# Kernel tuning notes

Measured on AMD Instinct MI355X. Metric: run time of the kernel, lower is better.

## Reference

```python
import jax, jax.numpy as jnp
import numpy as np
from jax import lax

B, T, L = 2048, 80, 128


def setup_inputs() -> dict:
    key = jax.random.key(0)
    k1, k2, k3, k4, k5 = jax.random.split(key, 5)
    x = jax.random.normal(k1, (B, T, L), dtype=jnp.float32)  # emissions (model logits)
    y = jax.random.randint(k2, (B, T), 0, L)                 # gold tag sequence
    trans = jax.random.normal(k3, (L, L), dtype=jnp.float32) * 0.1
    start_trans = jax.random.normal(k4, (L,), dtype=jnp.float32) * 0.1
    end_trans = jax.random.normal(k5, (L,), dtype=jnp.float32) * 0.1
    return {"x": x, "trans": trans, "start_trans": start_trans,
            "end_trans": end_trans, "y": y}


def reference(x, trans, start_trans, end_trans, y):
    # Linear-chain CRF log-likelihood (TorchCRF semantics, mask = all ones).
    # x: [B,T,L] emissions, y: [B,T] gold tags. Returns [B] log-likelihoods.
    # --- numerator: score of the gold path ---
    emit = jnp.take_along_axis(x, y[..., None], axis=2).squeeze(-1).sum(axis=1)  # [B]
    tr = trans[y[:, :-1], y[:, 1:]].sum(axis=1)                                  # [B]
    numerator = start_trans[y[:, 0]] + emit + tr + end_trans[y[:, -1]]           # [B]
    # --- denominator: log-partition via forward algorithm (scan over time) ---
    alpha0 = start_trans[None, :] + x[:, 0]  # [B,L]
    xt = jnp.swapaxes(x, 0, 1)[1:]           # [T-1,B,L]

    def step(alpha, h_t):
        # alpha[b,i] + trans[i,j] -> logsumexp over i, then add emission h_t[b,j]
        a = jax.nn.logsumexp(alpha[:, :, None] + trans[None, :, :], axis=1) + h_t
        return a, None

    alpha, _ = lax.scan(step, alpha0, xt)
    log_z = jax.nn.logsumexp(alpha + end_trans[None, :], axis=1)  # [B]
    return numerator - log_z
```

## Files before the change

### kernel.cpp

```cpp
#include <hip/hip_runtime.h>
#include <math.h>


#define CRF_B 2048
#define CRF_T 80
#define CRF_L 128

typedef __attribute__((ext_vector_type(8))) short bf16x8_t;
typedef __attribute__((ext_vector_type(4))) float f32x4_t;

union bfrag { bf16x8_t v; unsigned u[4]; unsigned short s[8]; };

__device__ __forceinline__ unsigned pack2(float lo, float hi) {
    return (__float_as_uint(lo) >> 16) | (__float_as_uint(hi) & 0xFFFF0000u);
}
__device__ __forceinline__ unsigned short bft(float f) {
    return (unsigned short)(__float_as_uint(f) >> 16);
}

__global__ __launch_bounds__(64, 1) void crf_v4_kernel(
    const float* __restrict__ x,
    const float* __restrict__ trans,
    const float* __restrict__ start_trans,
    const float* __restrict__ end_trans,
    const int*   __restrict__ y,
    float* __restrict__ out)
{
    const int lane = threadIdx.x;
    const int q    = lane >> 4;
    const int n16  = lane & 15;
    const int row0 = blockIdx.x * 16;
    const int brow = row0 + n16;

    const float* xr = x + (size_t)brow * (CRF_T * CRF_L);

    const int* yb = y + brow * CRF_T;
    float nume = 0.f;
    #pragma unroll
    for (int i = 0; i < 20; ++i) {
        const int t  = 4 * i + q;
        const int yt = yb[t];
        nume += xr[t * CRF_L + yt];
        nume += (t < CRF_T - 1) ? trans[yt * CRF_L + yb[t + 1]] : end_trans[yt];
        if (t == 0) nume += start_trans[yt];
    }
    nume += __shfl_xor(nume, 16);
    nume += __shfl_xor(nume, 32);

    bfrag Af[8][4];
    #pragma unroll
    for (int mt = 0; mt < 8; ++mt) {
        const int m = 16 * mt + n16;
        #pragma unroll
        for (int kk = 0; kk < 4; ++kk) {
            #pragma unroll
            for (int j = 0; j < 8; ++j) {
                const int s = ((2 * kk + (j >> 2)) << 4) | (q << 2) | (j & 3);
                Af[mt][kk].s[j] = bft(__expf(trans[s * CRF_L + m]));
            }
        }
    }

    f32x4_t xA[8], xB[8];
    #pragma unroll
    for (int mt = 0; mt < 8; ++mt) {
        xA[mt] = *(const f32x4_t*)&xr[0 * CRF_L + 16 * mt + 4 * q];
        xB[mt] = *(const f32x4_t*)&xr[1 * CRF_L + 16 * mt + 4 * q];
    }

    bfrag   Bf[4];
    f32x4_t acc[8];
    float crun = 0.f, invM = 1.f;

    #pragma unroll
    for (int mt = 0; mt < 8; ++mt) {
        const f32x4_t st4 = *(const f32x4_t*)&start_trans[16 * mt + 4 * q];
        #pragma unroll
        for (int r = 0; r < 4; ++r)
            acc[mt][r] = __expf(st4[r] + xA[mt][r]);
    }
    #pragma unroll
    for (int mt = 0; mt < 8; ++mt) {
        Bf[mt >> 1].u[2 * (mt & 1) + 0] = pack2(acc[mt][0], acc[mt][1]);
        Bf[mt >> 1].u[2 * (mt & 1) + 1] = pack2(acc[mt][2], acc[mt][3]);
    }
    #pragma unroll
    for (int mt = 0; mt < 8; ++mt)
        xA[mt] = *(const f32x4_t*)&xr[2 * CRF_L + 16 * mt + 4 * q];

    auto step = [&](int t, f32x4_t (&xc)[8]) {
        #pragma unroll
        for (int mt = 0; mt < 8; ++mt) {
            f32x4_t a = {0.f, 0.f, 0.f, 0.f};
            #pragma unroll
            for (int kk = 0; kk < 4; ++kk)
                a = __builtin_amdgcn_mfma_f32_16x16x32_bf16(Af[mt][kk].v, Bf[kk].v, a, 0, 0, 0);
            acc[mt] = a;
        }
        const bool ap = (t & 3) == 0;
        #pragma unroll
        for (int mt = 0; mt < 8; ++mt) {
            #pragma unroll
            for (int r = 0; r < 4; ++r) {
                float e = __expf(xc[mt][r]);
                if (ap) e *= invM;
                acc[mt][r] *= e;
            }
        }
        if (((t & 3) == 3) && (t < CRF_T - 1)) {
            float m = acc[0][0];
            #pragma unroll
            for (int mt = 0; mt < 8; ++mt)
                #pragma unroll
                for (int r = 0; r < 4; ++r)
                    m = fmaxf(m, acc[mt][r]);
            m = fmaxf(m, __shfl_xor(m, 16));
            m = fmaxf(m, __shfl_xor(m, 32));
            crun += __logf(m);
            invM  = 1.0f / m;
        }
        if (t < CRF_T - 1) {
            #pragma unroll
            for (int mt = 0; mt < 8; ++mt) {
                Bf[mt >> 1].u[2 * (mt & 1) + 0] = pack2(acc[mt][0], acc[mt][1]);
                Bf[mt >> 1].u[2 * (mt & 1) + 1] = pack2(acc[mt][2], acc[mt][3]);
            }
        }
        if (t + 2 < CRF_T) {
            #pragma unroll
            for (int mt = 0; mt < 8; ++mt)
                xc[mt] = *(const f32x4_t*)&xr[(t + 2) * CRF_L + 16 * mt + 4 * q];
        }
    };

    for (int tb = 1; tb + 1 < CRF_T; tb += 2) {
        step(tb,     xB);
        step(tb + 1, xA);
    }
    step(CRF_T - 1, xB);

    float sv = 0.f;
    #pragma unroll
    for (int mt = 0; mt < 8; ++mt) {
        const f32x4_t e4 = *(const f32x4_t*)&end_trans[16 * mt + 4 * q];
        #pragma unroll
        for (int r = 0; r < 4; ++r)
            sv += acc[mt][r] * __expf(e4[r]);
    }
    sv += __shfl_xor(sv, 16);
    sv += __shfl_xor(sv, 32);
    if (lane < 16) out[row0 + n16] = nume - (crun + __logf(sv));
}

extern "C" void kernel_launch(void* const* d_in, const int* in_sizes, int n_in,
                              void* d_out, int out_size, void* d_ws, size_t ws_size,
                              hipStream_t stream) {
    const float* x     = (const float*)d_in[0];
    const float* trans = (const float*)d_in[1];
    const float* st    = (const float*)d_in[2];
    const float* et    = (const float*)d_in[3];
    const int*   y     = (const int*)d_in[4];
    float* out = (float*)d_out;

    crf_v4_kernel<<<CRF_B / 16, 64, 0, stream>>>(x, trans, st, et, y, out);
}
```

Before: 187.8 us.

## Run forward and backward CRF recursions concurrently and meet in the middle

Splits the 80-step forward recursion into a forward chain from the start and a backward chain from the end, each about 40 steps, run together in the same wavefront and combined at the midpoint with one extra matrix product. This halves the serial dependency chain of MFMA-then-exp steps and gives the scheduler two independent chains to interleave, hiding MFMA latency. In exchange it doubles the register-resident transition fragments (forward and transposed) and the x prefetch buffers, which raises register pressure, and it adds a final combine step.

Result: slower. 265.2 us (+41.2%).

```diff
diff --git a/kernel.cpp b/kernel.cpp
--- a/kernel.cpp
+++ b/kernel.cpp
@@ -18,7 +18,7 @@
     return (unsigned short)(__float_as_uint(f) >> 16);
 }
 
-__global__ __launch_bounds__(64, 1) void crf_v4_kernel(
+__global__ __launch_bounds__(64, 1) void crf_v5_kernel(
     const float* __restrict__ x,
     const float* __restrict__ trans,
     const float* __restrict__ start_trans,
@@ -33,8 +33,8 @@
     const int brow = row0 + n16;
 
     const float* xr = x + (size_t)brow * (CRF_T * CRF_L);
-
-    const int* yb = y + brow * CRF_T;
+    const int*   yb = y + brow * CRF_T;
+
     float nume = 0.f;
     #pragma unroll
     for (int i = 0; i < 20; ++i) {
@@ -47,7 +47,7 @@
     nume += __shfl_xor(nume, 16);
     nume += __shfl_xor(nume, 32);
 
-    bfrag Af[8][4];
+    bfrag Aff[8][4], Afb[8][4];
     #pragma unroll
     for (int mt = 0; mt < 8; ++mt) {
         const int m = 16 * mt + n16;
@@ -56,100 +56,164 @@
             #pragma unroll
             for (int j = 0; j < 8; ++j) {
                 const int s = ((2 * kk + (j >> 2)) << 4) | (q << 2) | (j & 3);
-                Af[mt][kk].s[j] = bft(__expf(trans[s * CRF_L + m]));
-            }
-        }
-    }
-
-    f32x4_t xA[8], xB[8];
-    #pragma unroll
-    for (int mt = 0; mt < 8; ++mt) {
-        xA[mt] = *(const f32x4_t*)&xr[0 * CRF_L + 16 * mt + 4 * q];
-        xB[mt] = *(const f32x4_t*)&xr[1 * CRF_L + 16 * mt + 4 * q];
-    }
-
-    bfrag   Bf[4];
-    f32x4_t acc[8];
-    float crun = 0.f, invM = 1.f;
-
-    #pragma unroll
-    for (int mt = 0; mt < 8; ++mt) {
-        const f32x4_t st4 = *(const f32x4_t*)&start_trans[16 * mt + 4 * q];
-        #pragma unroll
-        for (int r = 0; r < 4; ++r)
-            acc[mt][r] = __expf(st4[r] + xA[mt][r]);
-    }
-    #pragma unroll
-    for (int mt = 0; mt < 8; ++mt) {
-        Bf[mt >> 1].u[2 * (mt & 1) + 0] = pack2(acc[mt][0], acc[mt][1]);
-        Bf[mt >> 1].u[2 * (mt & 1) + 1] = pack2(acc[mt][2], acc[mt][3]);
-    }
-    #pragma unroll
-    for (int mt = 0; mt < 8; ++mt)
-        xA[mt] = *(const f32x4_t*)&xr[2 * CRF_L + 16 * mt + 4 * q];
-
-    auto step = [&](int t, f32x4_t (&xc)[8]) {
-        #pragma unroll
-        for (int mt = 0; mt < 8; ++mt) {
-            f32x4_t a = {0.f, 0.f, 0.f, 0.f};
-            #pragma unroll
-            for (int kk = 0; kk < 4; ++kk)
-                a = __builtin_amdgcn_mfma_f32_16x16x32_bf16(Af[mt][kk].v, Bf[kk].v, a, 0, 0, 0);
-            acc[mt] = a;
-        }
-        const bool ap = (t & 3) == 0;
-        #pragma unroll
-        for (int mt = 0; mt < 8; ++mt) {
-            #pragma unroll
-            for (int r = 0; r < 4; ++r) {
-                float e = __expf(xc[mt][r]);
-                if (ap) e *= invM;
-                acc[mt][r] *= e;
-            }
-        }
-        if (((t & 3) == 3) && (t < CRF_T - 1)) {
-            float m = acc[0][0];
+                Aff[mt][kk].s[j] = bft(__expf(trans[s * CRF_L + m]));
+                Afb[mt][kk].s[j] = bft(__expf(trans[m * CRF_L + s]));
+            }
+        }
+    }
+
+    f32x4_t xF[2][8], xB[2][8], x0t[8], x9t[8];
+    #pragma unroll
+    for (int mt = 0; mt < 8; ++mt) {
+        const int c = 16 * mt + 4 * q;
+        x0t[mt]   = *(const f32x4_t*)&xr[ 0 * CRF_L + c];
+        x9t[mt]   = *(const f32x4_t*)&xr[79 * CRF_L + c];
+        xF[1][mt] = *(const f32x4_t*)&xr[ 1 * CRF_L + c];
+        xF[0][mt] = *(const f32x4_t*)&xr[ 2 * CRF_L + c];
+        xB[1][mt] = *(const f32x4_t*)&xr[78 * CRF_L + c];
+        xB[0][mt] = *(const f32x4_t*)&xr[77 * CRF_L + c];
+    }
+
+    bfrag BfF[4], BfB[4];
+    f32x4_t accF[8], accB[8];
+    float crunF = 0.f, crunB = 0.f, invF = 1.f, invB = 1.f;
+
+    #pragma unroll
+    for (int mt = 0; mt < 8; ++mt) {
+        const int c = 16 * mt + 4 * q;
+        const f32x4_t st4 = *(const f32x4_t*)&start_trans[c];
+        const f32x4_t en4 = *(const f32x4_t*)&end_trans[c];
+        #pragma unroll
+        for (int r = 0; r < 4; ++r) {
+            accF[mt][r] = __expf(st4[r] + x0t[mt][r]);
+            accB[mt][r] = __expf(en4[r] + x9t[mt][r]);
+        }
+    }
+    #pragma unroll
+    for (int mt = 0; mt < 8; ++mt) {
+        BfF[mt >> 1].u[2 * (mt & 1) + 0] = pack2(accF[mt][0], accF[mt][1]);
+        BfF[mt >> 1].u[2 * (mt & 1) + 1] = pack2(accF[mt][2], accF[mt][3]);
+        BfB[mt >> 1].u[2 * (mt & 1) + 0] = pack2(accB[mt][0], accB[mt][1]);
+        BfB[mt >> 1].u[2 * (mt & 1) + 1] = pack2(accB[mt][2], accB[mt][3]);
+    }
+
+    auto pairstep = [&](int k, f32x4_t (&xf)[8], f32x4_t (&xb)[8]) {
+        #pragma unroll
+        for (int mt = 0; mt < 8; ++mt) {
+            f32x4_t aF = {0.f, 0.f, 0.f, 0.f};
+            f32x4_t aB = {0.f, 0.f, 0.f, 0.f};
+            #pragma unroll
+            for (int kk = 0; kk < 4; ++kk) {
+                aF = __builtin_amdgcn_mfma_f32_16x16x32_bf16(Aff[mt][kk].v, BfF[kk].v, aF, 0, 0, 0);
+                aB = __builtin_amdgcn_mfma_f32_16x16x32_bf16(Afb[mt][kk].v, BfB[kk].v, aB, 0, 0, 0);
+            }
+            accF[mt] = aF;
+            accB[mt] = aB;
+        }
+        const bool ap = (k & 3) == 0;
+        #pragma unroll
+        for (int mt = 0; mt < 8; ++mt) {
+            #pragma unroll
+            for (int r = 0; r < 4; ++r) {
+                float eF = __expf(xf[mt][r]);
+                float eB = __expf(xb[mt][r]);
+                if (ap) { eF *= invF; eB *= invB; }
+                accF[mt][r] *= eF;
+                accB[mt][r] *= eB;
+            }
+        }
+        if (((k & 3) == 3) && (k < 39)) {
+            float mF = accF[0][0], mB = accB[0][0];
             #pragma unroll
             for (int mt = 0; mt < 8; ++mt)
                 #pragma unroll
-                for (int r = 0; r < 4; ++r)
-                    m = fmaxf(m, acc[mt][r]);
-            m = fmaxf(m, __shfl_xor(m, 16));
-            m = fmaxf(m, __shfl_xor(m, 32));
-            crun += __logf(m);
-            invM  = 1.0f / m;
-        }
-        if (t < CRF_T - 1) {
-            #pragma unroll
-            for (int mt = 0; mt < 8; ++mt) {
-                Bf[mt >> 1].u[2 * (mt & 1) + 0] = pack2(acc[mt][0], acc[mt][1]);
-                Bf[mt >> 1].u[2 * (mt & 1) + 1] = pack2(acc[mt][2], acc[mt][3]);
-            }
-        }
-        if (t + 2 < CRF_T) {
+                for (int r = 0; r < 4; ++r) {
+                    mF = fmaxf(mF, accF[mt][r]);
+                    mB = fmaxf(mB, accB[mt][r]);
+                }
+            mF = fmaxf(mF, __shfl_xor(mF, 16)); mF = fmaxf(mF, __shfl_xor(mF, 32));
+            mB = fmaxf(mB, __shfl_xor(mB, 16)); mB = fmaxf(mB, __shfl_xor(mB, 32));
+            crunF += __logf(mF); invF = 1.0f / mF;
+            crunB += __logf(mB); invB = 1.0f / mB;
+        }
+        #pragma unroll
+        for (int mt = 0; mt < 8; ++mt) {
+            BfF[mt >> 1].u[2 * (mt & 1) + 0] = pack2(accF[mt][0], accF[mt][1]);
+            BfF[mt >> 1].u[2 * (mt & 1) + 1] = pack2(accF[mt][2], accF[mt][3]);
+            BfB[mt >> 1].u[2 * (mt & 1) + 0] = pack2(accB[mt][0], accB[mt][1]);
+            BfB[mt >> 1].u[2 * (mt & 1) + 1] = pack2(accB[mt][2], accB[mt][3]);
+        }
+        if (k + 2 <= 39) {
             #pragma unroll
             for (int mt = 0; mt < 8; ++mt)
-                xc[mt] = *(const f32x4_t*)&xr[(t + 2) * CRF_L + 16 * mt + 4 * q];
+                xf[mt] = *(const f32x4_t*)&xr[(k + 2) * CRF_L + 16 * mt + 4 * q];
+        }
+        if (k <= 37) {
+            #pragma unroll
+            for (int mt = 0; mt < 8; ++mt)
+                xb[mt] = *(const f32x4_t*)&xr[(77 - k) * CRF_L + 16 * mt + 4 * q];
         }
     };
 
-    for (int tb = 1; tb + 1 < CRF_T; tb += 2) {
-        step(tb,     xB);
-        step(tb + 1, xA);
-    }
-    step(CRF_T - 1, xB);
+    for (int k = 1; k <= 37; k += 2) {
+        pairstep(k,     xF[1], xB[1]);
+        pairstep(k + 1, xF[0], xB[0]);
+    }
+
+    {
+        #pragma unroll
+        for (int mt = 0; mt < 8; ++mt) {
+            f32x4_t aF = {0.f, 0.f, 0.f, 0.f};
+            f32x4_t aB = {0.f, 0.f, 0.f, 0.f};
+            #pragma unroll
+            for (int kk = 0; kk < 4; ++kk) {
+                aF = __builtin_amdgcn_mfma_f32_16x16x32_bf16(Aff[mt][kk].v, BfF[kk].v, aF, 0, 0, 0);
+                aB = __builtin_amdgcn_mfma_f32_16x16x32_bf16(Afb[mt][kk].v, BfB[kk].v, aB, 0, 0, 0);
+            }
+            #pragma unroll
+            for (int r = 0; r < 4; ++r) {
+                accF[mt][r] = aF[r] * __expf(xF[1][mt][r]);
+                accB[mt][r] = aB[r] * __expf(xB[1][mt][r]);
+            }
+        }
+        float mF = accF[0][0], mB = accB[0][0];
+        #pragma unroll
+        for (int mt = 0; mt < 8; ++mt)
+            #pragma unroll
+            for (int r = 0; r < 4; ++r) {
+                mF = fmaxf(mF, accF[mt][r]);
+                mB = fmaxf(mB, accB[mt][r]);
+            }
+        mF = fmaxf(mF, __shfl_xor(mF, 16)); mF = fmaxf(mF, __shfl_xor(mF, 32));
+        mB = fmaxf(mB, __shfl_xor(mB, 16)); mB = fmaxf(mB, __shfl_xor(mB, 32));
+        crunF += __logf(mF); const float iF = 1.0f / mF;
+        crunB += __logf(mB); const float iB = 1.0f / mB;
+        #pragma unroll
+        for (int mt = 0; mt < 8; ++mt) {
+            #pragma unroll
+            for (int r = 0; r < 4; ++r) {
+                accF[mt][r] *= iF;
+                accB[mt][r] *= iB;
+            }
+            BfF[mt >> 1].u[2 * (mt & 1) + 0] = pack2(accF[mt][0], accF[mt][1]);
+            BfF[mt >> 1].u[2 * (mt & 1) + 1] = pack2(accF[mt][2], accF[mt][3]);
+        }
+    }
 
     float sv = 0.f;
     #pragma unroll
     for (int mt = 0; mt < 8; ++mt) {
-        const f32x4_t e4 = *(const f32x4_t*)&end_trans[16 * mt + 4 * q];
+        f32x4_t aF = {0.f, 0.f, 0.f, 0.f};
+        #pragma unroll
+        for (int kk = 0; kk < 4; ++kk)
+            aF = __builtin_amdgcn_mfma_f32_16x16x32_bf16(Aff[mt][kk].v, BfF[kk].v, aF, 0, 0, 0);
         #pragma unroll
         for (int r = 0; r < 4; ++r)
-            sv += acc[mt][r] * __expf(e4[r]);
+            sv += aF[r] * accB[mt][r];
     }
     sv += __shfl_xor(sv, 16);
     sv += __shfl_xor(sv, 32);
-    if (lane < 16) out[row0 + n16] = nume - (crun + __logf(sv));
+    if (lane < 16) out[row0 + n16] = nume - (crunF + crunB + __logf(sv));
 }
 
 extern "C" void kernel_launch(void* const* d_in, const int* in_sizes, int n_in,
@@ -162,5 +226,5 @@
     const int*   y     = (const int*)d_in[4];
     float* out = (float*)d_out;
 
-    crf_v4_kernel<<<CRF_B / 16, 64, 0, stream>>>(x, trans, st, et, y, out);
-}
+    crf_v5_kernel<<<CRF_B / 16, 64, 0, stream>>>(x, trans, st, et, y, out);
+}
```
